# Optimization experiments

Hardware: AMD Instinct MI355X
Metric: run time of the kernel (lower is better)

Reference implementation:

```python
import jax, jax.numpy as jnp
import numpy as np

TAU = 0.5  # temperature from init_kwargs


def _semi_loss(h1, h2):
    # GRACE-style InfoNCE: -log( e^{sim(i,i')/tau} / (sum_refl + sum_between - e^{sim(i,i)/tau}) )
    n1 = h1 / jnp.linalg.norm(h1, axis=1, keepdims=True)
    n2 = h2 / jnp.linalg.norm(h2, axis=1, keepdims=True)
    refl = jnp.exp((n1 @ n1.T) / TAU)   # [N, N]
    betw = jnp.exp((n1 @ n2.T) / TAU)   # [N, N]
    denom = refl.sum(axis=1) + betw.sum(axis=1) - jnp.diagonal(refl)
    return -jnp.log(jnp.diagonal(betw) / denom)


def _contrast(h1, h2):
    # forward_v1 with batch_size=0 (batched path is mathematically identical)
    return (0.5 * (_semi_loss(h1, h2) + _semi_loss(h2, h1))).mean()


def _proj(z, Wa, ba, Wb, bb):
    # fc_b(elu(fc_a(z))); torch Linear: y = x @ W.T + b
    return jax.nn.elu(z @ Wa.T + ba) @ Wb.T + bb


def setup_inputs() -> dict:
    key = jax.random.key(0)
    ks = jax.random.split(key, 11)
    N, A, B = 8192, 32, 32
    D = A * B
    s = 1.0 / np.sqrt(D)
    inp = {
        'ta': jax.random.normal(ks[0], (N, A, B), dtype=jnp.float32),
        'tb': jax.random.normal(ks[1], (N, A, B), dtype=jnp.float32),
        'W1': jax.random.uniform(ks[2], (D, D), jnp.float32, -s, s),
        'b1': jax.random.uniform(ks[3], (D,), jnp.float32, -s, s),
        'W2': jax.random.uniform(ks[4], (D, D), jnp.float32, -s, s),
        'b2': jax.random.uniform(ks[5], (D,), jnp.float32, -s, s),
        'W3': jax.random.uniform(ks[6], (D, D), jnp.float32, -s, s),
        'b3': jax.random.uniform(ks[7], (D,), jnp.float32, -s, s),
        'W4': jax.random.uniform(ks[8], (D, D), jnp.float32, -s, s),
        'b4': jax.random.uniform(ks[9], (D,), jnp.float32, -s, s),
        'w_r1': jnp.array([0.5], dtype=jnp.float32),
    }
    return inp


def reference(ta, tb, W1, b1, W2, b2, W3, b3, W4, b4, w_r1):
    N = ta.shape[0]
    # row view: [N, A*B]
    z1 = ta.reshape(N, -1)
    z2 = tb.reshape(N, -1)
    loss_row = _contrast(_proj(z1, W1, b1, W2, b2), _proj(z2, W1, b1, W2, b2))
    # column view: permute(0,2,1) then flatten -> [N, B*A]
    z1c = jnp.transpose(ta, (0, 2, 1)).reshape(N, -1)
    z2c = jnp.transpose(tb, (0, 2, 1)).reshape(N, -1)
    loss_col = _contrast(_proj(z1c, W3, b3, W4, b4), _proj(z2c, W3, b3, W4, b4))
    w_row = jnp.clip(w_r1[0], 0.0, 1.0)
    return w_row * loss_row + (1.0 - w_row) * loss_col
```

## Files before the change

### kernel.cpp

```cpp
#include <hip/hip_runtime.h>
#include <stdint.h>


typedef unsigned short u16;
typedef __attribute__((ext_vector_type(8))) __bf16 bf16x8;
typedef __attribute__((ext_vector_type(4))) float f32x4;

#define NS 8192
#define DD 1024

__device__ __forceinline__ float bf2f(u16 u) {
    union { uint32_t i; float f; } v; v.i = ((uint32_t)u) << 16; return v.f;
}
__device__ __forceinline__ u16 f2bf(float f) {
    union { float f; uint32_t i; } v; v.f = f;
    return (u16)((v.i + 0x7FFFu + ((v.i >> 16) & 1u)) >> 16);
}

__device__ __forceinline__ void gload16(const u16* g, u16* l) {
    __builtin_amdgcn_global_load_lds(
        (__attribute__((address_space(1))) void*)(uintptr_t)(g),
        (__attribute__((address_space(3))) void*)(uintptr_t)(l), 16, 0, 0);
}


__global__ __launch_bounds__(256) void conv_f2bf4(const float* __restrict__ W1,
                                                  const float* __restrict__ W2,
                                                  const float* __restrict__ W3,
                                                  const float* __restrict__ W4,
                                                  u16* __restrict__ dst) {
    const int b = blockIdx.x;
    const float* src = (b < 1024) ? W1 : (b < 2048) ? W2 : (b < 3072) ? W3 : W4;
    const size_t so = ((size_t)(b & 1023) << 10) + threadIdx.x * 4;
    const size_t dо = ((size_t)b << 10) + threadIdx.x * 4;
    float4 v = *(const float4*)(src + so);
    ushort4 o;
    o.x = f2bf(v.x); o.y = f2bf(v.y); o.z = f2bf(v.z); o.w = f2bf(v.w);
    *(ushort4*)(dst + dо) = o;
}

__global__ __launch_bounds__(256) void conv_cat(const float* __restrict__ a,
                                                const float* __restrict__ b,
                                                u16* __restrict__ Z) {
    size_t i = (size_t)(blockIdx.x * 256 + threadIdx.x) * 4;
    const size_t half = (size_t)NS * DD;
    const float* s = (i < half) ? (a + i) : (b + (i - half));
    float4 v = *(const float4*)s;
    ushort4 o;
    o.x = f2bf(v.x); o.y = f2bf(v.y); o.z = f2bf(v.z); o.w = f2bf(v.w);
    *(ushort4*)(Z + i) = o;
}

__global__ __launch_bounds__(256) void conv_col(const float* __restrict__ a,
                                                const float* __restrict__ b,
                                                u16* __restrict__ Z) {
    size_t i = (size_t)(blockIdx.x * 256 + threadIdx.x) * 4;
    const size_t half = (size_t)NS * DD;
    const float* src; size_t o;
    if (i < half) { src = a; o = i; } else { src = b; o = i - half; }
    size_t row = o >> 10;
    int j = (int)(o & 1023);
    int aI = j & 31, bI = j >> 5;
    const float* rp = src + (row << 10);
    ushort4 ov;
    ov.x = f2bf(rp[aI * 32 + bI]);
    ov.y = f2bf(rp[(aI + 1) * 32 + bI]);
    ov.z = f2bf(rp[(aI + 2) * 32 + bI]);
    ov.w = f2bf(rp[(aI + 3) * 32 + bI]);
    *(ushort4*)(Z + i) = ov;
}

template <int MODE>
__global__ __launch_bounds__(256) void gemm_bt(const u16* A, const u16* B,
                                               const float* __restrict__ bias,
                                               u16* __restrict__ out) {
    __shared__ alignas(16) u16 As[128 * 32];
    __shared__ alignas(16) u16 Bs[128 * 32];
    const int tid = threadIdx.x;

    const int tm = blockIdx.y, tn = blockIdx.x;
    const size_t tileM = (size_t)tm * 128;
    const size_t tileN = (size_t)tn * 128;

    const int csw = ((tid & 3) ^ ((tid >> 4) & 3)) * 8;
    const u16* gA0 = A + (tileM + (tid >> 2)) * DD + csw;
    const u16* gA1 = gA0 + (size_t)64 * DD;
    const u16* gB0 = B + (tileN + (tid >> 2)) * DD + csw;
    const u16* gB1 = gB0 + (size_t)64 * DD;
    u16* lA0 = &As[tid * 8]; u16* lA1 = lA0 + 2048;
    u16* lB0 = &Bs[tid * 8]; u16* lB1 = lB0 + 2048;

    const int lane = tid & 63;
    const int wv = tid >> 6;
    const int wr = (wv >> 1) << 6;
    const int wc = (wv & 1) << 6;
    const int lr = lane & 15;
    const int lh = lane >> 4;
    const int sw = lh ^ ((lr >> 2) & 3);

    const u16* aBase = &As[(wr + lr) * 32 + sw * 8];
    const u16* bBase = &Bs[(wc + lr) * 32 + sw * 8];

    f32x4 acc[4][4];
#pragma unroll
    for (int i = 0; i < 4; i++)
#pragma unroll
        for (int j = 0; j < 4; j++) acc[i][j] = (f32x4)0.0f;

    for (int k0 = 0; k0 < DD; k0 += 32) {
        gload16(gA0 + k0, lA0);
        gload16(gA1 + k0, lA1);
        gload16(gB0 + k0, lB0);
        gload16(gB1 + k0, lB1);
        __syncthreads();
        bf16x8 af[4], bfr[4];
#pragma unroll
        for (int rt = 0; rt < 4; rt++) af[rt] = *(const bf16x8*)(aBase + rt * 512);
#pragma unroll
        for (int ct = 0; ct < 4; ct++) bfr[ct] = *(const bf16x8*)(bBase + ct * 512);
#pragma unroll
        for (int rt = 0; rt < 4; rt++)
#pragma unroll
            for (int ct = 0; ct < 4; ct++)
                acc[rt][ct] = __builtin_amdgcn_mfma_f32_16x16x32_bf16(
                    af[rt], bfr[ct], acc[rt][ct], 0, 0, 0);
        __syncthreads();
    }

    float bcol[4];
#pragma unroll
    for (int ct = 0; ct < 4; ct++) bcol[ct] = bias[tileN + wc + ct * 16 + lr];
#pragma unroll
    for (int rt = 0; rt < 4; rt++) {
#pragma unroll
        for (int r = 0; r < 4; r++) {
            size_t row = tileM + wr + rt * 16 + lh * 4 + r;
            u16* orow = out + row * DD + tileN + wc + lr;
#pragma unroll
            for (int ct = 0; ct < 4; ct++) {
                float v = acc[rt][ct][r] + bcol[ct];
                if (MODE == 0) v = v > 0.0f ? v : expm1f(v);
                orow[ct * 16] = f2bf(v);
            }
        }
    }
}

__global__ __launch_bounds__(512, 2) void gram256(const u16* __restrict__ Hr,
                                                  const u16* __restrict__ Hc,
                                                  float* __restrict__ Sbase) {
    __shared__ alignas(16) u16 LA[4][256 * 32];
    __shared__ alignas(16) u16 LB[4][256 * 32];
    const int tid = threadIdx.x;

    const int view = (int)blockIdx.y >> 5;
    const u16* H = view ? Hc : Hr;
    float* S = Sbase + view * 2 * NS;
    int x = blockIdx.x, y = (int)blockIdx.y & 31;
    int tm, tn;
    if (y + x < 64) { tm = y;      tn = y + x; }
    else            { tm = 63 - y; tn = x - 1; }

    const size_t rowA = (size_t)tm * 256;
    const size_t rowB = (size_t)tn * 256;

    const int r_lo = tid >> 2;
    const int csw  = ((tid & 3) ^ ((r_lo >> 2) & 3)) * 8;
    const u16* gA0 = H + (rowA + r_lo) * DD + csw;
    const u16* gA1 = H + (rowA + 128 + r_lo) * DD + csw;
    const u16* gB0 = H + (rowB + r_lo) * DD + csw;
    const u16* gB1 = H + (rowB + 128 + r_lo) * DD + csw;
    const int ldst = tid * 8;

    const int lane = tid & 63;
    const int wv = tid >> 6;
    const int wr = (wv >> 2) * 128;
    const int wc = (wv & 3) * 64;
    const int lr = lane & 15;
    const int lh = lane >> 4;
    const int sw = lh ^ ((lr >> 2) & 3);
    const int aoff = (wr + lr) * 32 + sw * 8;
    const int boff = (wc + lr) * 32 + sw * 8;

    f32x4 acc[8][4];
#pragma unroll
    for (int i = 0; i < 8; ++i)
#pragma unroll
        for (int j = 0; j < 4; ++j) acc[i][j] = (f32x4)0.0f;

#pragma unroll
    for (int t = 0; t < 3; ++t) {
        const int k0 = t * 32;
        gload16(gA0 + k0, &LA[t][0] + ldst);
        gload16(gA1 + k0, &LA[t][4096] + ldst);
        gload16(gB0 + k0, &LB[t][0] + ldst);
        gload16(gB1 + k0, &LB[t][4096] + ldst);
    }

    for (int t = 0; t < 32; ++t) {
        if (t < 30)       asm volatile("s_waitcnt vmcnt(8)" ::: "memory");
        else if (t == 30) asm volatile("s_waitcnt vmcnt(4)" ::: "memory");
        else              asm volatile("s_waitcnt vmcnt(0)" ::: "memory");
        __builtin_amdgcn_s_barrier();
        asm volatile("" ::: "memory");

        const int buf = t & 3;
        const u16* la = &LA[buf][0];
        const u16* lb = &LB[buf][0];

        bf16x8 bF[4], aF[8];
#pragma unroll
        for (int i = 0; i < 4; ++i) bF[i] = *(const bf16x8*)(lb + boff + i * 512);
#pragma unroll
        for (int i = 0; i < 8; ++i) aF[i] = *(const bf16x8*)(la + aoff + i * 512);

        if (t < 29) {
            const int nbuf = (t + 3) & 3;
            const int k0n = (t + 3) * 32;
            gload16(gA0 + k0n, &LA[nbuf][0] + ldst);
            gload16(gA1 + k0n, &LA[nbuf][4096] + ldst);
            gload16(gB0 + k0n, &LB[nbuf][0] + ldst);
            gload16(gB1 + k0n, &LB[nbuf][4096] + ldst);
        }

        __builtin_amdgcn_s_setprio(1);
#pragma unroll
        for (int mi = 0; mi < 8; ++mi)
#pragma unroll
            for (int ni = 0; ni < 4; ++ni)
                acc[mi][ni] = __builtin_amdgcn_mfma_f32_16x16x32_bf16(
                    aF[mi], bF[ni], acc[mi][ni], 0, 0, 0);
        __builtin_amdgcn_s_setprio(0);
    }

    const bool offdiag = (tm != tn);
    float colsum[4] = {0.f, 0.f, 0.f, 0.f};
#pragma unroll
    for (int q = 0; q < 8; ++q) {
#pragma unroll
        for (int r = 0; r < 4; ++r) {
            float rs = 0.0f;
#pragma unroll
            for (int ni = 0; ni < 4; ++ni) {
                float e = __expf(2.0f * acc[q][ni][r]);
                rs += e;
                colsum[ni] += e;
            }
            rs += __shfl_xor(rs, 1);
            rs += __shfl_xor(rs, 2);
            rs += __shfl_xor(rs, 4);
            rs += __shfl_xor(rs, 8);
            if (lr == 0) {
                size_t row = rowA + wr + q * 16 + lh * 4 + r;
                atomicAdd(&S[row], rs);
            }
        }
    }
    if (offdiag) {
#pragma unroll
        for (int ni = 0; ni < 4; ++ni) {
            float cs = colsum[ni];
            cs += __shfl_xor(cs, 16);
            cs += __shfl_xor(cs, 32);
            if (lh == 0) {
                size_t col = rowB + wc + ni * 16 + lr;
                atomicAdd(&S[col], cs);
            }
        }
    }
}

__global__ __launch_bounds__(256) void normdiag_kernel(u16* M, float* g12) {
    __shared__ float red[12];
    const int tid = threadIdx.x;
    u16* r1 = M + ((size_t)blockIdx.x << 10);
    u16* r2 = r1 + ((size_t)NS << 10);
    ushort4 va = ((const ushort4*)r1)[tid];
    ushort4 vb = ((const ushort4*)r2)[tid];
    float a0 = bf2f(va.x), a1 = bf2f(va.y), a2 = bf2f(va.z), a3 = bf2f(va.w);
    float b0 = bf2f(vb.x), b1 = bf2f(vb.y), b2 = bf2f(vb.z), b3 = bf2f(vb.w);
    float s1 = a0 * a0 + a1 * a1 + a2 * a2 + a3 * a3;
    float s2 = b0 * b0 + b1 * b1 + b2 * b2 + b3 * b3;
#pragma unroll
    for (int m = 1; m < 64; m <<= 1) {
        s1 += __shfl_xor(s1, m);
        s2 += __shfl_xor(s2, m);
    }
    const int w = tid >> 6;
    if ((tid & 63) == 0) { red[w] = s1; red[4 + w] = s2; }
    __syncthreads();
    float inv1 = rsqrtf(red[0] + red[1] + red[2] + red[3]);
    float inv2 = rsqrtf(red[4] + red[5] + red[6] + red[7]);
    ushort4 oa, ob;
    oa.x = f2bf(a0 * inv1); oa.y = f2bf(a1 * inv1);
    oa.z = f2bf(a2 * inv1); oa.w = f2bf(a3 * inv1);
    ob.x = f2bf(b0 * inv2); ob.y = f2bf(b1 * inv2);
    ob.z = f2bf(b2 * inv2); ob.w = f2bf(b3 * inv2);
    ((ushort4*)r1)[tid] = oa;
    ((ushort4*)r2)[tid] = ob;
    float d = bf2f(oa.x) * bf2f(ob.x) + bf2f(oa.y) * bf2f(ob.y) +
              bf2f(oa.z) * bf2f(ob.z) + bf2f(oa.w) * bf2f(ob.w);
#pragma unroll
    for (int m = 1; m < 64; m <<= 1) d += __shfl_xor(d, m);
    if ((tid & 63) == 0) red[8 + w] = d;
    __syncthreads();
    if (tid == 0) g12[blockIdx.x] = red[8] + red[9] + red[10] + red[11];
}

__global__ __launch_bounds__(256) void final_kernel(const float* Sr, const float* Sc,
                                                    const float* gr, const float* gc,
                                                    const float* w_r1, float* out) {
    __shared__ float red[16];
    const float E2 = 7.389056098930650f;
    float a = 0.f, b = 0.f, c = 0.f, d = 0.f;
    for (int i = threadIdx.x; i < 2 * NS; i += 256) {
        a += logf(Sr[i] - E2);
        b += logf(Sc[i] - E2);
    }
    for (int i = threadIdx.x; i < NS; i += 256) {
        c += gr[i];
        d += gc[i];
    }
#pragma unroll
    for (int m = 1; m < 64; m <<= 1) {
        a += __shfl_xor(a, m); b += __shfl_xor(b, m);
        c += __shfl_xor(c, m); d += __shfl_xor(d, m);
    }
    int w = threadIdx.x >> 6;
    if ((threadIdx.x & 63) == 0) {
        red[w] = a; red[4 + w] = b; red[8 + w] = c; red[12 + w] = d;
    }
    __syncthreads();
    if (threadIdx.x == 0) {
        a = red[0] + red[1] + red[2] + red[3];
        b = red[4] + red[5] + red[6] + red[7];
        c = red[8] + red[9] + red[10] + red[11];
        d = red[12] + red[13] + red[14] + red[15];
        float lr = a / (2.0f * NS) - 2.0f * c / NS;
        float lc = b / (2.0f * NS) - 2.0f * d / NS;
        float w0 = w_r1[0];
        w0 = fminf(fmaxf(w0, 0.0f), 1.0f);
        out[0] = w0 * lr + (1.0f - w0) * lc;
    }
}

extern "C" void kernel_launch(void* const* d_in, const int* in_sizes, int n_in,
                              void* d_out, int out_size, void* d_ws, size_t ws_size,
                              hipStream_t stream) {
    const float* ta = (const float*)d_in[0];
    const float* tb = (const float*)d_in[1];
    const float* W1 = (const float*)d_in[2];
    const float* b1 = (const float*)d_in[3];
    const float* W2 = (const float*)d_in[4];
    const float* b2 = (const float*)d_in[5];
    const float* W3 = (const float*)d_in[6];
    const float* b3 = (const float*)d_in[7];
    const float* W4 = (const float*)d_in[8];
    const float* b4 = (const float*)d_in[9];
    const float* wr = (const float*)d_in[10];
    float* out = (float*)d_out;

    char* p = (char*)d_ws;
    const size_t MAT = (size_t)2 * NS * DD * sizeof(u16);
    u16* Z = (u16*)p;  p += MAT;
    u16* T = (u16*)p;  p += MAT;
    u16* H = (u16*)p;  p += MAT;
    u16* Wb = (u16*)p; p += (size_t)4 * DD * DD * sizeof(u16);
    float* Sr = (float*)p;  p += 2 * NS * sizeof(float);
    float* Sc = (float*)p;  p += 2 * NS * sizeof(float);
    float* gr = (float*)p;  p += NS * sizeof(float);
    float* gc = (float*)p;  p += NS * sizeof(float);

    u16* Wb1 = Wb;
    u16* Wb2 = Wb + (size_t)DD * DD;
    u16* Wb3 = Wb + (size_t)2 * DD * DD;
    u16* Wb4 = Wb + (size_t)3 * DD * DD;

    conv_f2bf4<<<4096, 256, 0, stream>>>(W1, W2, W3, W4, Wb);
    hipMemsetAsync(Sr, 0, 4 * NS * sizeof(float), stream);

    conv_cat<<<16384, 256, 0, stream>>>(ta, tb, Z);
    gemm_bt<0><<<dim3(8, 128), 256, 0, stream>>>(Z, Wb1, b1, T);
    gemm_bt<1><<<dim3(8, 128), 256, 0, stream>>>(T, Wb2, b2, H);
    normdiag_kernel<<<8192, 256, 0, stream>>>(H, gr);

    conv_col<<<16384, 256, 0, stream>>>(ta, tb, Z);
    gemm_bt<0><<<dim3(8, 128), 256, 0, stream>>>(Z, Wb3, b3, T);
    gemm_bt<1><<<dim3(8, 128), 256, 0, stream>>>(T, Wb4, b4, Z);
    normdiag_kernel<<<8192, 256, 0, stream>>>(Z, gc);

    gram256<<<dim3(65, 64), 512, 0, stream>>>(H, Z, Sr);

    final_kernel<<<1, 256, 0, stream>>>(Sr, Sc, gr, gc, wr, out);
}
```

Before: 1.124 ms.

## Replace projection GEMM with 256x256-tile, 4-stage pipelined async-LDS kernel

The four projection GEMMs move from a 128x128 tile kernel with one sync-bounded stage per K step to a 256x256 tile kernel using 512 threads, a 4-deep LDS ring buffer with three K-slices prefetched, explicit vmcnt waits, and raised priority around the MFMA block. The aim is to hide global load latency behind compute and raise operand reuse per LDS load. In exchange each block uses more registers and LDS, and the grid shrinks to 256 blocks, which may leave compute units underused. A variable with a non-ASCII name in the weight conversion kernel is also renamed.

Result: faster. 1.085 ms (-3.4%).

```diff
diff --git a/kernel.cpp b/kernel.cpp
--- a/kernel.cpp
+++ b/kernel.cpp
@@ -32,11 +32,11 @@
     const int b = blockIdx.x;
     const float* src = (b < 1024) ? W1 : (b < 2048) ? W2 : (b < 3072) ? W3 : W4;
     const size_t so = ((size_t)(b & 1023) << 10) + threadIdx.x * 4;
-    const size_t dо = ((size_t)b << 10) + threadIdx.x * 4;
+    const size_t doo = ((size_t)b << 10) + threadIdx.x * 4;
     float4 v = *(const float4*)(src + so);
     ushort4 o;
     o.x = f2bf(v.x); o.y = f2bf(v.y); o.z = f2bf(v.z); o.w = f2bf(v.w);
-    *(ushort4*)(dst + dо) = o;
+    *(ushort4*)(dst + doo) = o;
 }
 
 __global__ __launch_bounds__(256) void conv_cat(const float* __restrict__ a,
@@ -71,76 +71,100 @@
 }
 
 template <int MODE>
-__global__ __launch_bounds__(256) void gemm_bt(const u16* A, const u16* B,
-                                               const float* __restrict__ bias,
-                                               u16* __restrict__ out) {
-    __shared__ alignas(16) u16 As[128 * 32];
-    __shared__ alignas(16) u16 Bs[128 * 32];
+__global__ __launch_bounds__(512, 2) void gemm256_bt(const u16* __restrict__ A,
+                                                     const u16* __restrict__ B,
+                                                     const float* __restrict__ bias,
+                                                     u16* __restrict__ out) {
+    __shared__ alignas(16) u16 LA[4][256 * 32];
+    __shared__ alignas(16) u16 LB[4][256 * 32];
     const int tid = threadIdx.x;
 
-    const int tm = blockIdx.y, tn = blockIdx.x;
-    const size_t tileM = (size_t)tm * 128;
-    const size_t tileN = (size_t)tn * 128;
-
-    const int csw = ((tid & 3) ^ ((tid >> 4) & 3)) * 8;
-    const u16* gA0 = A + (tileM + (tid >> 2)) * DD + csw;
-    const u16* gA1 = gA0 + (size_t)64 * DD;
-    const u16* gB0 = B + (tileN + (tid >> 2)) * DD + csw;
-    const u16* gB1 = gB0 + (size_t)64 * DD;
-    u16* lA0 = &As[tid * 8]; u16* lA1 = lA0 + 2048;
-    u16* lB0 = &Bs[tid * 8]; u16* lB1 = lB0 + 2048;
+    const size_t rowA = (size_t)blockIdx.y * 256;
+    const size_t rowB = (size_t)blockIdx.x * 256;
+
+    const int r_lo = tid >> 2;
+    const int csw  = ((tid & 3) ^ ((r_lo >> 2) & 3)) * 8;
+    const u16* gA0 = A + (rowA + r_lo) * DD + csw;
+    const u16* gA1 = A + (rowA + 128 + r_lo) * DD + csw;
+    const u16* gB0 = B + (rowB + r_lo) * DD + csw;
+    const u16* gB1 = B + (rowB + 128 + r_lo) * DD + csw;
+    const int ldst = tid * 8;
 
     const int lane = tid & 63;
     const int wv = tid >> 6;
-    const int wr = (wv >> 1) << 6;
-    const int wc = (wv & 1) << 6;
+    const int wr = (wv >> 2) * 128;
+    const int wc = (wv & 3) * 64;
     const int lr = lane & 15;
     const int lh = lane >> 4;
     const int sw = lh ^ ((lr >> 2) & 3);
-
-    const u16* aBase = &As[(wr + lr) * 32 + sw * 8];
-    const u16* bBase = &Bs[(wc + lr) * 32 + sw * 8];
-
-    f32x4 acc[4][4];
-#pragma unroll
-    for (int i = 0; i < 4; i++)
-#pragma unroll
-        for (int j = 0; j < 4; j++) acc[i][j] = (f32x4)0.0f;
-
-    for (int k0 = 0; k0 < DD; k0 += 32) {
-        gload16(gA0 + k0, lA0);
-        gload16(gA1 + k0, lA1);
-        gload16(gB0 + k0, lB0);
-        gload16(gB1 + k0, lB1);
-        __syncthreads();
-        bf16x8 af[4], bfr[4];
-#pragma unroll
-        for (int rt = 0; rt < 4; rt++) af[rt] = *(const bf16x8*)(aBase + rt * 512);
-#pragma unroll
-        for (int ct = 0; ct < 4; ct++) bfr[ct] = *(const bf16x8*)(bBase + ct * 512);
-#pragma unroll
-        for (int rt = 0; rt < 4; rt++)
-#pragma unroll
-            for (int ct = 0; ct < 4; ct++)
-                acc[rt][ct] = __builtin_amdgcn_mfma_f32_16x16x32_bf16(
-                    af[rt], bfr[ct], acc[rt][ct], 0, 0, 0);
-        __syncthreads();
+    const int aoff = (wr + lr) * 32 + sw * 8;
+    const int boff = (wc + lr) * 32 + sw * 8;
+
+    f32x4 acc[8][4];
+#pragma unroll
+    for (int i = 0; i < 8; ++i)
+#pragma unroll
+        for (int j = 0; j < 4; ++j) acc[i][j] = (f32x4)0.0f;
+
+#pragma unroll
+    for (int t = 0; t < 3; ++t) {
+        const int k0 = t * 32;
+        gload16(gA0 + k0, &LA[t][0] + ldst);
+        gload16(gA1 + k0, &LA[t][4096] + ldst);
+        gload16(gB0 + k0, &LB[t][0] + ldst);
+        gload16(gB1 + k0, &LB[t][4096] + ldst);
+    }
+
+    for (int t = 0; t < 32; ++t) {
+        if (t < 30)       asm volatile("s_waitcnt vmcnt(8)" ::: "memory");
+        else if (t == 30) asm volatile("s_waitcnt vmcnt(4)" ::: "memory");
+        else              asm volatile("s_waitcnt vmcnt(0)" ::: "memory");
+        __builtin_amdgcn_s_barrier();
+        asm volatile("" ::: "memory");
+
+        const int buf = t & 3;
+        const u16* la = &LA[buf][0];
+        const u16* lb = &LB[buf][0];
+
+        bf16x8 bF[4], aF[8];
+#pragma unroll
+        for (int i = 0; i < 4; ++i) bF[i] = *(const bf16x8*)(lb + boff + i * 512);
+#pragma unroll
+        for (int i = 0; i < 8; ++i) aF[i] = *(const bf16x8*)(la + aoff + i * 512);
+
+        if (t < 29) {
+            const int nbuf = (t + 3) & 3;
+            const int k0n = (t + 3) * 32;
+            gload16(gA0 + k0n, &LA[nbuf][0] + ldst);
+            gload16(gA1 + k0n, &LA[nbuf][4096] + ldst);
+            gload16(gB0 + k0n, &LB[nbuf][0] + ldst);
+            gload16(gB1 + k0n, &LB[nbuf][4096] + ldst);
+        }
+
+        __builtin_amdgcn_s_setprio(1);
+#pragma unroll
+        for (int mi = 0; mi < 8; ++mi)
+#pragma unroll
+            for (int ni = 0; ni < 4; ++ni)
+                acc[mi][ni] = __builtin_amdgcn_mfma_f32_16x16x32_bf16(
+                    aF[mi], bF[ni], acc[mi][ni], 0, 0, 0);
+        __builtin_amdgcn_s_setprio(0);
     }
 
     float bcol[4];
 #pragma unroll
-    for (int ct = 0; ct < 4; ct++) bcol[ct] = bias[tileN + wc + ct * 16 + lr];
-#pragma unroll
-    for (int rt = 0; rt < 4; rt++) {
-#pragma unroll
-        for (int r = 0; r < 4; r++) {
-            size_t row = tileM + wr + rt * 16 + lh * 4 + r;
-            u16* orow = out + row * DD + tileN + wc + lr;
-#pragma unroll
-            for (int ct = 0; ct < 4; ct++) {
-                float v = acc[rt][ct][r] + bcol[ct];
+    for (int ni = 0; ni < 4; ++ni) bcol[ni] = bias[rowB + wc + ni * 16 + lr];
+#pragma unroll
+    for (int q = 0; q < 8; ++q) {
+#pragma unroll
+        for (int r = 0; r < 4; ++r) {
+            size_t row = rowA + wr + q * 16 + lh * 4 + r;
+            u16* orow = out + row * DD + rowB + wc + lr;
+#pragma unroll
+            for (int ni = 0; ni < 4; ++ni) {
+                float v = acc[q][ni][r] + bcol[ni];
                 if (MODE == 0) v = v > 0.0f ? v : expm1f(v);
-                orow[ct * 16] = f2bf(v);
+                orow[ni * 16] = f2bf(v);
             }
         }
     }
@@ -380,13 +404,13 @@
     hipMemsetAsync(Sr, 0, 4 * NS * sizeof(float), stream);
 
     conv_cat<<<16384, 256, 0, stream>>>(ta, tb, Z);
-    gemm_bt<0><<<dim3(8, 128), 256, 0, stream>>>(Z, Wb1, b1, T);
-    gemm_bt<1><<<dim3(8, 128), 256, 0, stream>>>(T, Wb2, b2, H);
+    gemm256_bt<0><<<dim3(4, 64), 512, 0, stream>>>(Z, Wb1, b1, T);
+    gemm256_bt<1><<<dim3(4, 64), 512, 0, stream>>>(T, Wb2, b2, H);
     normdiag_kernel<<<8192, 256, 0, stream>>>(H, gr);
 
     conv_col<<<16384, 256, 0, stream>>>(ta, tb, Z);
-    gemm_bt<0><<<dim3(8, 128), 256, 0, stream>>>(Z, Wb3, b3, T);
-    gemm_bt<1><<<dim3(8, 128), 256, 0, stream>>>(T, Wb4, b4, Z);
+    gemm256_bt<0><<<dim3(4, 64), 512, 0, stream>>>(Z, Wb3, b3, T);
+    gemm256_bt<1><<<dim3(4, 64), 512, 0, stream>>>(T, Wb4, b4, Z);
     normdiag_kernel<<<8192, 256, 0, stream>>>(Z, gc);
 
     gram256<<<dim3(65, 64), 512, 0, stream>>>(H, Z, Sr);
```
